# Kernel tuning notes

Measured on AMD Instinct MI355X. Metric: run time of the kernel, lower is better.

Reference implementation:

```python
import jax, jax.numpy as jnp
import numpy as np

# Tree: 64 leaves (16 feat -> 16 out), 8 mids (16 feat + 8*16 child = 144 -> 32 out),
# root (16 feat + 8*32 child = 272 -> 64 out), head -> 10 tasks. Eval-mode BatchNorm.
B = 16384
EPS = 1e-5


def setup_inputs() -> dict:
    key = jax.random.key(0)
    ks = jax.random.split(key, 24)
    rn = lambda k, s: jax.random.normal(k, s, dtype=jnp.float32)
    ru = lambda k, s: jax.random.uniform(k, s, dtype=jnp.float32)
    return {
        "x": rn(ks[0], (B, 1168)),
        # leaf layers (64 nodes, 16 -> 16)
        "Wl": rn(ks[1], (64, 16, 16)) * 0.1, "bl": rn(ks[2], (64, 16)) * 0.1,
        "gl": ru(ks[3], (64, 16)) + 0.5, "betal": rn(ks[4], (64, 16)) * 0.1,
        "ml": rn(ks[5], (64, 16)) * 0.1, "vl": ru(ks[6], (64, 16)) + 0.5,
        # mid layers (8 nodes, 144 -> 32)
        "Wm": rn(ks[7], (8, 144, 32)) * 0.1, "bm": rn(ks[8], (8, 32)) * 0.1,
        "gm": ru(ks[9], (8, 32)) + 0.5, "betam": rn(ks[10], (8, 32)) * 0.1,
        "mm": rn(ks[11], (8, 32)) * 0.1, "vm": ru(ks[12], (8, 32)) + 0.5,
        # root layer (272 -> 64)
        "Wr": rn(ks[13], (272, 64)) * 0.1, "br": rn(ks[14], (64,)) * 0.1,
        "gr": ru(ks[15], (64,)) + 0.5, "betar": rn(ks[16], (64,)) * 0.1,
        "mr": rn(ks[17], (64,)) * 0.1, "vr": ru(ks[18], (64,)) + 0.5,
        # root prediction head (64 -> 10 tasks)
        "Wh": rn(ks[19], (64, 10)) * 0.1, "bh": rn(ks[20], (10,)) * 0.1,
    }


def _bn(h, g, b, m, v):
    return (h - m) * jax.lax.rsqrt(v + EPS) * g + b


def reference(x, Wl, bl, gl, betal, ml, vl, Wm, bm, gm, betam, mm, vm,
              Wr, br, gr, betar, mr, vr, Wh, bh):
    n = x.shape[0]
    # leaves: gather own features (contiguous layout), Linear+BN+Tanh, batched over 64 nodes
    xl = x[:, :1024].reshape(n, 64, 16)
    hl = jnp.tanh(_bn(jnp.einsum('bli,lio->blo', xl, Wl) + bl, gl, betal, ml, vl))
    # mids: concat own features with 8 leaf-child outputs -> [n, 8, 144]
    xm = x[:, 1024:1152].reshape(n, 8, 16)
    mid_in = jnp.concatenate([xm, hl.reshape(n, 8, 128)], axis=-1)
    hm = jnp.tanh(_bn(jnp.einsum('bmi,mio->bmo', mid_in, Wm) + bm, gm, betam, mm, vm))
    # root: concat own features with 8 mid outputs -> [n, 272]
    root_in = jnp.concatenate([x[:, 1152:1168], hm.reshape(n, 256)], axis=-1)
    hr = jnp.tanh(_bn(root_in @ Wr + br, gr, betar, mr, vr))
    # root prediction head (eval-mode forward returns only root prediction)
    return hr @ Wh + bh
```

## Files before the change

kernel.cpp:

```cpp
#include <hip/hip_runtime.h>
#include <hip/hip_bf16.h>

typedef __attribute__((ext_vector_type(8))) short bf16x8;
typedef __attribute__((ext_vector_type(4))) float f32x4;

#define EPS 1e-5f
#define K2L 2.8853900817779268f

#define N_FRAG_BLOCKS 182
#define WSB_LEAF 0
#define WSB_MID  64
#define WSB_ROOT 144
#define WSB_HEAD 180
#define ST_SL 0
#define ST_TL 1024
#define ST_SM 2048
#define ST_TM 2304
#define ST_SR 2560
#define ST_TR 2624
#define WS_ST_BYTE_OFF (N_FRAG_BLOCKS * 1024)

__device__ __forceinline__ unsigned short f2bf(float f) {
    unsigned u = __float_as_uint(f);
    unsigned r = u + 0x7fffu + ((u >> 16) & 1u);
    return (unsigned short)(r >> 16);
}

__device__ __forceinline__ unsigned pk2(float a, float b) {
    float2 f2; f2.x = a; f2.y = b;
    __hip_bfloat162 h = __float22bfloat162_rn(f2);
    union { __hip_bfloat162 h2; unsigned u; } cv; cv.h2 = h;
    return cv.u;
}

__device__ __forceinline__ bf16x8 pack8(float4 a, float4 b) {
    union { unsigned u[4]; bf16x8 v; } r;
    r.u[0] = pk2(a.x, a.y); r.u[1] = pk2(a.z, a.w);
    r.u[2] = pk2(b.x, b.y); r.u[3] = pk2(b.z, b.w);
    return r.v;
}

__device__ __forceinline__ float bn_act(float acc, float Sp, float Tp) {
    float e = exp2f(fmaf(acc, Sp, Tp));
    float r = __builtin_amdgcn_rcpf(e + 1.0f);
    return fmaf(-2.0f, r, 1.0f);
}

__global__ void ontology_prep(
    const float* __restrict__ Wl, const float* __restrict__ Wm,
    const float* __restrict__ Wr, const float* __restrict__ Wh,
    const float* __restrict__ bl, const float* __restrict__ gl,
    const float* __restrict__ betal, const float* __restrict__ ml,
    const float* __restrict__ vl,
    const float* __restrict__ bm, const float* __restrict__ gm,
    const float* __restrict__ betam, const float* __restrict__ mm,
    const float* __restrict__ vm,
    const float* __restrict__ br, const float* __restrict__ gr,
    const float* __restrict__ betar, const float* __restrict__ mr,
    const float* __restrict__ vr,
    unsigned short* __restrict__ wsFrag, float* __restrict__ wsST)
{
    const int b = blockIdx.x;
    const int t = threadIdx.x;
    if (b < N_FRAG_BLOCKS) {
        const int row = t & 15, g = t >> 4;
        unsigned short vals[8];
        #pragma unroll
        for (int i = 0; i < 8; ++i) {
            const int k = g * 8 + i;
            float v = 0.f;
            if (b < 64) {
                const int l = b;
                if ((l & 1) == 0) { if (k < 16)  v = Wl[l * 256 + k * 16 + row]; }
                else              { if (k >= 16) v = Wl[l * 256 + (k - 16) * 16 + row]; }
            } else if (b < 144) {
                const int idx = b - 64, m = idx / 10, rem = idx % 10;
                const int tt = rem / 5, s = rem % 5;
                const int krow = s * 32 + k;
                if (krow < 144) v = Wm[m * 4608 + krow * 32 + tt * 16 + row];
            } else if (b < 180) {
                const int idx = b - 144, tt = idx / 9, s = idx % 9;
                if (s == 0) { if (k < 16) v = Wr[k * 64 + tt * 16 + row]; }
                else { const int krow = 16 + (s - 1) * 32 + k;
                       v = Wr[krow * 64 + tt * 16 + row]; }
            } else {
                const int s = b - 180, krow = s * 32 + k;
                if (row < 10) v = Wh[krow * 10 + row];
            }
            vals[i] = f2bf(v);
        }
        #pragma unroll
        for (int i = 0; i < 8; ++i) wsFrag[b * 512 + t * 8 + i] = vals[i];
    } else if (b == N_FRAG_BLOCKS) {
        for (int i = 0; i < 16; ++i) {
            const int id = t + 64 * i;
            const float S = gl[id] * rsqrtf(vl[id] + EPS);
            wsST[ST_SL + id] = S * K2L;
            wsST[ST_TL + id] = ((bl[id] - ml[id]) * S + betal[id]) * K2L;
        }
    } else if (b == N_FRAG_BLOCKS + 1) {
        for (int i = 0; i < 4; ++i) {
            const int id = t + 64 * i;
            const float S = gm[id] * rsqrtf(vm[id] + EPS);
            wsST[ST_SM + id] = S * K2L;
            wsST[ST_TM + id] = ((bm[id] - mm[id]) * S + betam[id]) * K2L;
        }
    } else {
        const int id = t;
        const float S = gr[id] * rsqrtf(vr[id] + EPS);
        wsST[ST_SR + id] = S * K2L;
        wsST[ST_TR + id] = ((br[id] - mr[id]) * S + betar[id]) * K2L;
    }
}

__global__ __launch_bounds__(512, 8) void ontology_mfma(
    const float* __restrict__ x,
    const unsigned short* __restrict__ wsFrag,
    const float* __restrict__ wsST,
    const float* __restrict__ bh,
    float* __restrict__ out)
{
    __shared__ __align__(16) unsigned short lds[8 * 2560];

    const int tid  = threadIdx.x;
    const int w    = tid >> 6;
    const int lane = tid & 63;
    const int c    = lane & 15;
    const int g    = lane >> 4;
    const int rowbase = blockIdx.x * 16;
    const float* xrow = x + (size_t)(rowbase + c) * 1168;

    unsigned short* my = lds + w * 2560;
    unsigned short* hr = lds + 7 * 2560 + 1280;

    const float* Sl = wsST + ST_SL; const float* Tl = wsST + ST_TL;
    const float* Sm = wsST + ST_SM; const float* Tm = wsST + ST_TM;
    const float* Sr = wsST + ST_SR; const float* Tr = wsST + ST_TR;

    { uint2 z; z.x = 0u; z.y = 0u;
      *(uint2*)(my + c * 160 + 144 + 4 * g) = z; }

    {
        float4 xm4 = *(const float4*)(xrow + 1024 + w * 16 + 4 * g);
        uint2 pm; pm.x = pk2(xm4.x, xm4.y); pm.y = pk2(xm4.z, xm4.w);
        *(uint2*)(my + c * 160 + 4 * g) = pm;
    }

    #pragma unroll
    for (int p = 0; p < 4; ++p) {
        const float* a = xrow + (w * 4 + p) * 32 + g * 8;
        float4 xa = *(const float4*)a;
        float4 x2 = *(const float4*)(a + 4);
        bf16x8 bfrag = pack8(xa, x2);
        #pragma unroll
        for (int e = 0; e < 2; ++e) {
            const int l = 2 * p + e, leaf = w * 8 + l;
            bf16x8 afrag = *(const bf16x8*)(wsFrag + (WSB_LEAF + leaf) * 512 + lane * 8);
            f32x4 zz = {0.f,0.f,0.f,0.f};
            f32x4 acc = __builtin_amdgcn_mfma_f32_16x16x32_bf16(afrag, bfrag, zz, 0, 0, 0);
            const int po = leaf * 16 + 4 * g;
            float4 S = *(const float4*)(Sl + po);
            float4 T = *(const float4*)(Tl + po);
            uint2 pk;
            pk.x = pk2(bn_act(acc[0], S.x, T.x), bn_act(acc[1], S.y, T.y));
            pk.y = pk2(bn_act(acc[2], S.z, T.z), bn_act(acc[3], S.w, T.w));
            *(uint2*)(my + c * 160 + 16 + l * 16 + 4 * g) = pk;
        }
    }

    {
        f32x4 acc0 = {0.f,0.f,0.f,0.f};
        f32x4 acc1 = {0.f,0.f,0.f,0.f};
        const unsigned short* fb = wsFrag + (WSB_MID + w * 10) * 512 + lane * 8;
        #pragma unroll
        for (int s = 0; s < 5; ++s) {
            bf16x8 bfrag = *(const bf16x8*)(my + c * 160 + s * 32 + g * 8);
            bf16x8 a0 = *(const bf16x8*)(fb + s * 512);
            bf16x8 a1 = *(const bf16x8*)(fb + (5 + s) * 512);
            acc0 = __builtin_amdgcn_mfma_f32_16x16x32_bf16(a0, bfrag, acc0, 0, 0, 0);
            acc1 = __builtin_amdgcn_mfma_f32_16x16x32_bf16(a1, bfrag, acc1, 0, 0, 0);
        }
        #pragma unroll
        for (int tt = 0; tt < 2; ++tt) {
            f32x4 acc = tt ? acc1 : acc0;
            const int po = w * 32 + tt * 16 + 4 * g;
            float4 S = *(const float4*)(Sm + po);
            float4 T = *(const float4*)(Tm + po);
            uint2 pk;
            pk.x = pk2(bn_act(acc[0], S.x, T.x), bn_act(acc[1], S.y, T.y));
            pk.y = pk2(bn_act(acc[2], S.z, T.z), bn_act(acc[3], S.w, T.w));
            *(uint2*)(my + c * 40 + tt * 16 + 4 * g) = pk;
        }
    }

    __syncthreads();

    if (w < 4) {
        const unsigned short* fb = wsFrag + (WSB_ROOT + w * 9) * 512 + lane * 8;
        f32x4 acc = {0.f,0.f,0.f,0.f};
        {
            const float* rp = xrow + 1152 + (g & 1) * 8;
            float4 xrA = *(const float4*)rp;
            float4 xrB = *(const float4*)(rp + 4);
            bf16x8 bfrag = pack8(xrA, xrB);
            bf16x8 a0 = *(const bf16x8*)fb;
            acc = __builtin_amdgcn_mfma_f32_16x16x32_bf16(a0, bfrag, acc, 0, 0, 0);
        }
        #pragma unroll
        for (int s = 1; s <= 8; ++s) {
            bf16x8 bfrag = *(const bf16x8*)(lds + (s - 1) * 2560 + c * 40 + g * 8);
            bf16x8 a0 = *(const bf16x8*)(fb + s * 512);
            acc = __builtin_amdgcn_mfma_f32_16x16x32_bf16(a0, bfrag, acc, 0, 0, 0);
        }
        const int po = w * 16 + 4 * g;
        float4 S = *(const float4*)(Sr + po);
        float4 T = *(const float4*)(Tr + po);
        uint2 pk;
        pk.x = pk2(bn_act(acc[0], S.x, T.x), bn_act(acc[1], S.y, T.y));
        pk.y = pk2(bn_act(acc[2], S.z, T.z), bn_act(acc[3], S.w, T.w));
        *(uint2*)(hr + c * 72 + w * 16 + 4 * g) = pk;
    }

    __syncthreads();

    if (w == 0) {
        f32x4 acc = {0.f,0.f,0.f,0.f};
        #pragma unroll
        for (int s = 0; s < 2; ++s) {
            bf16x8 bfrag = *(const bf16x8*)(hr + c * 72 + s * 32 + g * 8);
            bf16x8 a0 = *(const bf16x8*)(wsFrag + (WSB_HEAD + s) * 512 + lane * 8);
            acc = __builtin_amdgcn_mfma_f32_16x16x32_bf16(a0, bfrag, acc, 0, 0, 0);
        }
        float* op = out + (size_t)(rowbase + c) * 10 + 4 * g;
        if (g < 2) {
            float2 o1 = {acc[0] + bh[4 * g],     acc[1] + bh[4 * g + 1]};
            float2 o2 = {acc[2] + bh[4 * g + 2], acc[3] + bh[4 * g + 3]};
            *(float2*)op = o1;
            *(float2*)(op + 2) = o2;
        } else if (g == 2) {
            float2 o1 = {acc[0] + bh[8], acc[1] + bh[9]};
            *(float2*)op = o1;
        }
    }
}

extern "C" void kernel_launch(void* const* d_in, const int* in_sizes, int n_in,
                              void* d_out, int out_size, void* d_ws, size_t ws_size,
                              hipStream_t stream) {
    const float* x     = (const float*)d_in[0];
    const float* Wl    = (const float*)d_in[1];
    const float* bl    = (const float*)d_in[2];
    const float* gl    = (const float*)d_in[3];
    const float* betal = (const float*)d_in[4];
    const float* ml    = (const float*)d_in[5];
    const float* vl    = (const float*)d_in[6];
    const float* Wm    = (const float*)d_in[7];
    const float* bm    = (const float*)d_in[8];
    const float* gm    = (const float*)d_in[9];
    const float* betam = (const float*)d_in[10];
    const float* mm    = (const float*)d_in[11];
    const float* vm    = (const float*)d_in[12];
    const float* Wr    = (const float*)d_in[13];
    const float* br    = (const float*)d_in[14];
    const float* gr    = (const float*)d_in[15];
    const float* betar = (const float*)d_in[16];
    const float* mr    = (const float*)d_in[17];
    const float* vr    = (const float*)d_in[18];
    const float* Wh    = (const float*)d_in[19];
    const float* bh    = (const float*)d_in[20];
    float* out = (float*)d_out;

    unsigned short* wsFrag = (unsigned short*)d_ws;
    float* wsST = (float*)((char*)d_ws + WS_ST_BYTE_OFF);

    ontology_prep<<<N_FRAG_BLOCKS + 3, 64, 0, stream>>>(
        Wl, Wm, Wr, Wh, bl, gl, betal, ml, vl, bm, gm, betam, mm, vm,
        br, gr, betar, mr, vr, wsFrag, wsST);

    const int n = in_sizes[0] / 1168;
    ontology_mfma<<<n / 16, 512, 0, stream>>>(x, wsFrag, wsST, bh, out);
}
```

Before: 32.36 us.

## Stage input tile into LDS with coalesced loads and reuse it for all stages

The main kernel now cooperatively loads the block's 16 contiguous input rows with fully coalesced float4 reads, converts them to bf16 once and keeps them in a single padded LDS tile. Leaf, mid, root and head outputs are written back into that same tile in place, and the mid weight fragments are reordered to match. This replaces the previous per-lane strided row reads, which touched a different 4.6KB row per lane. The prep kernel is also consolidated into fewer, larger blocks. The cost is an extra barrier before compute and more LDS per block, about 38KB against 40KB before.

```diff
diff --git a/kernel.cpp b/kernel.cpp
--- a/kernel.cpp
+++ b/kernel.cpp
@@ -20,6 +20,8 @@
 #define ST_TR 2624
 #define WS_ST_BYTE_OFF (N_FRAG_BLOCKS * 1024)
 
+#define XSW 1192
+
 __device__ __forceinline__ unsigned short f2bf(float f) {
     unsigned u = __float_as_uint(f);
     unsigned r = u + 0x7fffu + ((u >> 16) & 1u);
@@ -31,13 +33,6 @@
     __hip_bfloat162 h = __float22bfloat162_rn(f2);
     union { __hip_bfloat162 h2; unsigned u; } cv; cv.h2 = h;
     return cv.u;
-}
-
-__device__ __forceinline__ bf16x8 pack8(float4 a, float4 b) {
-    union { unsigned u[4]; bf16x8 v; } r;
-    r.u[0] = pk2(a.x, a.y); r.u[1] = pk2(a.z, a.w);
-    r.u[2] = pk2(b.x, b.y); r.u[3] = pk2(b.z, b.w);
-    return r.v;
 }
 
 __device__ __forceinline__ float bn_act(float acc, float Sp, float Tp) {
@@ -60,9 +55,11 @@
     const float* __restrict__ vr,
     unsigned short* __restrict__ wsFrag, float* __restrict__ wsST)
 {
-    const int b = blockIdx.x;
-    const int t = threadIdx.x;
-    if (b < N_FRAG_BLOCKS) {
+    const int tid = threadIdx.x;
+    if (blockIdx.x < 46) {
+        const int b = blockIdx.x * 4 + (tid >> 6);
+        if (b >= N_FRAG_BLOCKS) return;
+        const int t = tid & 63;
         const int row = t & 15, g = t >> 4;
         unsigned short vals[8];
         #pragma unroll
@@ -76,8 +73,9 @@
             } else if (b < 144) {
                 const int idx = b - 64, m = idx / 10, rem = idx % 10;
                 const int tt = rem / 5, s = rem % 5;
-                const int krow = s * 32 + k;
-                if (krow < 144) v = Wm[m * 4608 + krow * 32 + tt * 16 + row];
+                const int j = s * 32 + k;
+                const int krow = (j < 128) ? (16 + j) : ((j < 144) ? (j - 128) : -1);
+                if (krow >= 0) v = Wm[m * 4608 + krow * 32 + tt * 16 + row];
             } else if (b < 180) {
                 const int idx = b - 144, tt = idx / 9, s = idx % 9;
                 if (s == 0) { if (k < 16) v = Wr[k * 64 + tt * 16 + row]; }
@@ -91,25 +89,26 @@
         }
         #pragma unroll
         for (int i = 0; i < 8; ++i) wsFrag[b * 512 + t * 8 + i] = vals[i];
-    } else if (b == N_FRAG_BLOCKS) {
-        for (int i = 0; i < 16; ++i) {
-            const int id = t + 64 * i;
+    } else {
+        #pragma unroll
+        for (int i = 0; i < 4; ++i) {
+            const int id = tid + 256 * i;
             const float S = gl[id] * rsqrtf(vl[id] + EPS);
             wsST[ST_SL + id] = S * K2L;
             wsST[ST_TL + id] = ((bl[id] - ml[id]) * S + betal[id]) * K2L;
         }
-    } else if (b == N_FRAG_BLOCKS + 1) {
-        for (int i = 0; i < 4; ++i) {
-            const int id = t + 64 * i;
+        {
+            const int id = tid;
             const float S = gm[id] * rsqrtf(vm[id] + EPS);
             wsST[ST_SM + id] = S * K2L;
             wsST[ST_TM + id] = ((bm[id] - mm[id]) * S + betam[id]) * K2L;
         }
-    } else {
-        const int id = t;
-        const float S = gr[id] * rsqrtf(vr[id] + EPS);
-        wsST[ST_SR + id] = S * K2L;
-        wsST[ST_TR + id] = ((br[id] - mr[id]) * S + betar[id]) * K2L;
+        if (tid < 64) {
+            const int id = tid;
+            const float S = gr[id] * rsqrtf(vr[id] + EPS);
+            wsST[ST_SR + id] = S * K2L;
+            wsST[ST_TR + id] = ((br[id] - mr[id]) * S + betar[id]) * K2L;
+        }
     }
 }
 
@@ -120,7 +119,7 @@
     const float* __restrict__ bh,
     float* __restrict__ out)
 {
-    __shared__ __align__(16) unsigned short lds[8 * 2560];
+    __shared__ __align__(16) unsigned short xs[16 * XSW];
 
     const int tid  = threadIdx.x;
     const int w    = tid >> 6;
@@ -128,30 +127,44 @@
     const int c    = lane & 15;
     const int g    = lane >> 4;
     const int rowbase = blockIdx.x * 16;
-    const float* xrow = x + (size_t)(rowbase + c) * 1168;
-
-    unsigned short* my = lds + w * 2560;
-    unsigned short* hr = lds + 7 * 2560 + 1280;
 
     const float* Sl = wsST + ST_SL; const float* Tl = wsST + ST_TL;
     const float* Sm = wsST + ST_SM; const float* Tm = wsST + ST_TM;
     const float* Sr = wsST + ST_SR; const float* Tr = wsST + ST_TR;
 
-    { uint2 z; z.x = 0u; z.y = 0u;
-      *(uint2*)(my + c * 160 + 144 + 4 * g) = z; }
-
     {
-        float4 xm4 = *(const float4*)(xrow + 1024 + w * 16 + 4 * g);
-        uint2 pm; pm.x = pk2(xm4.x, xm4.y); pm.y = pk2(xm4.z, xm4.w);
-        *(uint2*)(my + c * 160 + 4 * g) = pm;
-    }
-
+        const float4* xt = (const float4*)(x + (size_t)rowbase * 1168);
+        #pragma unroll
+        for (int k = 0; k < 9; ++k) {
+            const int idx4 = k * 512 + tid;
+            float4 v = xt[idx4];
+            const int f = idx4 * 4;
+            const int row = f / 1168;
+            const int col = f - row * 1168;
+            uint2 p; p.x = pk2(v.x, v.y); p.y = pk2(v.z, v.w);
+            *(uint2*)(xs + row * XSW + col) = p;
+        }
+        if (tid < 64) {
+            const int idx4 = 4608 + tid;
+            float4 v = xt[idx4];
+            const int f = idx4 * 4;
+            const int row = f / 1168;
+            const int col = f - row * 1168;
+            uint2 p; p.x = pk2(v.x, v.y); p.y = pk2(v.z, v.w);
+            *(uint2*)(xs + row * XSW + col) = p;
+        }
+        if (tid < 64) {
+            const int row = tid >> 2, seg = tid & 3;
+            uint2 z; z.x = 0u; z.y = 0u;
+            *(uint2*)(xs + row * XSW + 1168 + seg * 4) = z;
+        }
+    }
+    __syncthreads();
+
+    const int colbase = w * 128;
     #pragma unroll
     for (int p = 0; p < 4; ++p) {
-        const float* a = xrow + (w * 4 + p) * 32 + g * 8;
-        float4 xa = *(const float4*)a;
-        float4 x2 = *(const float4*)(a + 4);
-        bf16x8 bfrag = pack8(xa, x2);
+        bf16x8 bfrag = *(const bf16x8*)(xs + c * XSW + colbase + p * 32 + g * 8);
         #pragma unroll
         for (int e = 0; e < 2; ++e) {
             const int l = 2 * p + e, leaf = w * 8 + l;
@@ -164,7 +177,7 @@
             uint2 pk;
             pk.x = pk2(bn_act(acc[0], S.x, T.x), bn_act(acc[1], S.y, T.y));
             pk.y = pk2(bn_act(acc[2], S.z, T.z), bn_act(acc[3], S.w, T.w));
-            *(uint2*)(my + c * 160 + 16 + l * 16 + 4 * g) = pk;
+            *(uint2*)(xs + c * XSW + colbase + l * 16 + 4 * g) = pk;
         }
     }
 
@@ -174,7 +187,8 @@
         const unsigned short* fb = wsFrag + (WSB_MID + w * 10) * 512 + lane * 8;
         #pragma unroll
         for (int s = 0; s < 5; ++s) {
-            bf16x8 bfrag = *(const bf16x8*)(my + c * 160 + s * 32 + g * 8);
+            const int cc = (s < 4) ? (colbase + s * 32) : (1024 + w * 16);
+            bf16x8 bfrag = *(const bf16x8*)(xs + c * XSW + cc + g * 8);
             bf16x8 a0 = *(const bf16x8*)(fb + s * 512);
             bf16x8 a1 = *(const bf16x8*)(fb + (5 + s) * 512);
             acc0 = __builtin_amdgcn_mfma_f32_16x16x32_bf16(a0, bfrag, acc0, 0, 0, 0);
@@ -189,26 +203,22 @@
             uint2 pk;
             pk.x = pk2(bn_act(acc[0], S.x, T.x), bn_act(acc[1], S.y, T.y));
             pk.y = pk2(bn_act(acc[2], S.z, T.z), bn_act(acc[3], S.w, T.w));
-            *(uint2*)(my + c * 40 + tt * 16 + 4 * g) = pk;
-        }
-    }
-
+            *(uint2*)(xs + c * XSW + colbase + tt * 16 + 4 * g) = pk;
+        }
+    }
     __syncthreads();
 
     if (w < 4) {
         const unsigned short* fb = wsFrag + (WSB_ROOT + w * 9) * 512 + lane * 8;
         f32x4 acc = {0.f,0.f,0.f,0.f};
         {
-            const float* rp = xrow + 1152 + (g & 1) * 8;
-            float4 xrA = *(const float4*)rp;
-            float4 xrB = *(const float4*)(rp + 4);
-            bf16x8 bfrag = pack8(xrA, xrB);
+            bf16x8 bfrag = *(const bf16x8*)(xs + c * XSW + 1152 + g * 8);
             bf16x8 a0 = *(const bf16x8*)fb;
             acc = __builtin_amdgcn_mfma_f32_16x16x32_bf16(a0, bfrag, acc, 0, 0, 0);
         }
         #pragma unroll
         for (int s = 1; s <= 8; ++s) {
-            bf16x8 bfrag = *(const bf16x8*)(lds + (s - 1) * 2560 + c * 40 + g * 8);
+            bf16x8 bfrag = *(const bf16x8*)(xs + c * XSW + (s - 1) * 128 + g * 8);
             bf16x8 a0 = *(const bf16x8*)(fb + s * 512);
             acc = __builtin_amdgcn_mfma_f32_16x16x32_bf16(a0, bfrag, acc, 0, 0, 0);
         }
@@ -218,16 +228,15 @@
         uint2 pk;
         pk.x = pk2(bn_act(acc[0], S.x, T.x), bn_act(acc[1], S.y, T.y));
         pk.y = pk2(bn_act(acc[2], S.z, T.z), bn_act(acc[3], S.w, T.w));
-        *(uint2*)(hr + c * 72 + w * 16 + 4 * g) = pk;
-    }
-
+        *(uint2*)(xs + c * XSW + 32 + w * 16 + 4 * g) = pk;
+    }
     __syncthreads();
 
     if (w == 0) {
         f32x4 acc = {0.f,0.f,0.f,0.f};
         #pragma unroll
         for (int s = 0; s < 2; ++s) {
-            bf16x8 bfrag = *(const bf16x8*)(hr + c * 72 + s * 32 + g * 8);
+            bf16x8 bfrag = *(const bf16x8*)(xs + c * XSW + 32 + s * 32 + g * 8);
             bf16x8 a0 = *(const bf16x8*)(wsFrag + (WSB_HEAD + s) * 512 + lane * 8);
             acc = __builtin_amdgcn_mfma_f32_16x16x32_bf16(a0, bfrag, acc, 0, 0, 0);
         }
@@ -273,7 +282,7 @@
     unsigned short* wsFrag = (unsigned short*)d_ws;
     float* wsST = (float*)((char*)d_ws + WS_ST_BYTE_OFF);
 
-    ontology_prep<<<N_FRAG_BLOCKS + 3, 64, 0, stream>>>(
+    ontology_prep<<<47, 256, 0, stream>>>(
         Wl, Wm, Wr, Wh, bl, gl, betal, ml, vl, bm, gm, betam, mm, vm,
         br, gr, betar, mr, vr, wsFrag, wsST);
 
```

After: 32.28 us. No clear change (-0.2%).
